# Optimization experiments

Measured on AMD Instinct MI355X. Metric: run time of the kernel, lower is better.

The kernel has to match this reference:

```python
import jax, jax.numpy as jnp
import numpy as np

N = 100000   # nodes
E = 1600000  # edges
F_IN = 256   # input features
H = 128      # hidden
C = 40       # classes


def setup_inputs() -> dict:
    key = jax.random.key(0)
    ks = jax.random.split(key, 6)
    x = jax.random.normal(ks[0], (N, F_IN), dtype=jnp.float32)
    edge_index = jax.random.randint(ks[1], (2, E), 0, N, dtype=jnp.int32)
    edge_attr = jax.random.uniform(ks[2], (E,), dtype=jnp.float32)
    # Glorot-style init like GCNConv
    W1 = jax.random.normal(ks[3], (F_IN, H), dtype=jnp.float32) * (1.0 / np.sqrt(F_IN))
    b1 = jnp.zeros((H,), dtype=jnp.float32)
    W2 = jax.random.normal(ks[4], (H, C), dtype=jnp.float32) * (1.0 / np.sqrt(H))
    b2 = jnp.zeros((C,), dtype=jnp.float32)
    return {"x": x, "edge_index": edge_index, "edge_attr": edge_attr,
            "W1": W1, "b1": b1, "W2": W2, "b2": b2}


def _gcn_norm(edge_index, edge_weight, num_nodes):
    # PyG gcn_norm: add self-loops (weight 1), symmetric D^{-1/2} A D^{-1/2}
    row, col = edge_index[0], edge_index[1]
    loop = jnp.arange(num_nodes, dtype=row.dtype)
    row = jnp.concatenate([row, loop])
    col = jnp.concatenate([col, loop])
    ew = jnp.concatenate([edge_weight, jnp.ones((num_nodes,), edge_weight.dtype)])
    deg = jax.ops.segment_sum(ew, col, num_segments=num_nodes)
    dinv = jnp.where(deg > 0, jax.lax.rsqrt(deg), 0.0)
    norm = dinv[row] * ew * dinv[col]
    return row, col, norm


def _gcn_conv(x, row, col, norm, W, b):
    h = x @ W                              # [N, out] dense transform first
    msg = h[row] * norm[:, None]           # gather source + edge scaling
    out = jax.ops.segment_sum(msg, col, num_segments=x.shape[0])  # scatter-add
    return out + b


def reference(x, edge_index, edge_attr, W1, b1, W2, b2):
    row, col, norm = _gcn_norm(edge_index, edge_attr, x.shape[0])
    h = _gcn_conv(x, row, col, norm, W1, b1)
    h = jax.nn.relu(h)
    # dropout is identity in eval mode
    h = _gcn_conv(h, row, col, norm, W2, b2)
    return jax.nn.log_softmax(h, axis=1)
```

## Files before the change

kernel.cpp:

```cpp
#include <hip/hip_runtime.h>

#define N_NODES 100000
#define N_EDGES 1600000
#define F_INPUT 256
#define H_DIM   128
#define C_DIM   40
#define NBKT    391
#define NCHK    1563
#define NMEGA   (2 * NCHK)

typedef short  bf8   __attribute__((ext_vector_type(8)));
typedef float  f32x4 __attribute__((ext_vector_type(4)));
typedef float  f32x2 __attribute__((ext_vector_type(2)));
typedef unsigned short u16x8 __attribute__((ext_vector_type(8)));

static __device__ __forceinline__ unsigned short f2bf(float f) {
    union { float f; unsigned u; } v; v.f = f;
    unsigned r = v.u + 0x7FFFu + ((v.u >> 16) & 1u);
    return (unsigned short)(r >> 16);
}
static __device__ __forceinline__ f32x2 bfpair(unsigned u) {
    union { unsigned u; float f; } lo, hi;
    lo.u = u << 16; hi.u = u & 0xFFFF0000u;
    return (f32x2){lo.f, hi.f};
}

__global__ void k_pre(const float* __restrict__ W1, const float* __restrict__ W2,
                      unsigned short* Wp1, unsigned short* Wp2) {
    int idx = blockIdx.x * 256 + threadIdx.x;
    if (idx < 32768) {
        int j = idx & 7, lane = (idx >> 3) & 63, ks = (idx >> 9) & 7, nt = idx >> 12;
        int m = lane & 15, q = lane >> 4;
        Wp1[idx] = f2bf(W1[(ks * 32 + q * 8 + j) * H_DIM + nt * 16 + m]);
    }
    int idx2 = idx - 32768;
    if (idx2 >= 0 && idx2 < 6144) {
        int j = idx2 & 7, lane = (idx2 >> 3) & 63, ks = (idx2 >> 9) & 3, nt = idx2 >> 11;
        int m = lane & 15, q = lane >> 4;
        int n = nt * 16 + m;
        Wp2[idx2] = (n < C_DIM) ? f2bf(W2[(ks * 32 + q * 8 + j) * C_DIM + n]) : (unsigned short)0;
    }
}

__global__ __launch_bounds__(256, 4) void k_mega2(
        const float* __restrict__ x, const unsigned short* __restrict__ Wp,
        unsigned short* __restrict__ h,
        const int* __restrict__ col, unsigned* __restrict__ histG) {
    __shared__ unsigned short lds_out[64 * H_DIM];
    int b = blockIdx.x;
    int tid = threadIdx.x;
    if (b & 1) {
        unsigned* histL = (unsigned*)lds_out;
        int chunk = b >> 1;
        for (int i = tid; i < NBKT; i += 256) histL[i] = 0;
        __syncthreads();
        int e0 = chunk * 1024 + tid;
#pragma unroll
        for (int k = 0; k < 4; k++) {
            int e = e0 + k * 256;
            if (e < N_EDGES) atomicAdd(&histL[col[e] >> 8], 1u);
        }
        __syncthreads();
        for (int i = tid; i < NBKT; i += 256) histG[(size_t)i * NCHK + chunk] = histL[i];
        return;
    }
    int tile = b >> 1;
    int wave = tid >> 6, lane = tid & 63;
    int m = lane & 15, q = lane >> 4;
    int row0 = tile * 64 + wave * 16;
    int rowA = row0 + m; if (rowA >= N_NODES) rowA = N_NODES - 1;

    f32x4 acc[8];
#pragma unroll
    for (int i = 0; i < 8; i++) acc[i] = (f32x4){0.f, 0.f, 0.f, 0.f};
    const float* xr = x + (long)rowA * F_INPUT + q * 8;
#pragma unroll
    for (int ks = 0; ks < 8; ks++) {
        float4 a0 = *(const float4*)(xr + ks * 32);
        float4 a1 = *(const float4*)(xr + ks * 32 + 4);
        bf8 a;
        a[0] = (short)f2bf(a0.x); a[1] = (short)f2bf(a0.y);
        a[2] = (short)f2bf(a0.z); a[3] = (short)f2bf(a0.w);
        a[4] = (short)f2bf(a1.x); a[5] = (short)f2bf(a1.y);
        a[6] = (short)f2bf(a1.z); a[7] = (short)f2bf(a1.w);
#pragma unroll
        for (int nt = 0; nt < 8; nt++) {
            bf8 bb = *(const bf8*)(Wp + (((nt * 8 + ks) * 64 + lane) << 3));
            acc[nt] = __builtin_amdgcn_mfma_f32_16x16x32_bf16(a, bb, acc[nt], 0, 0, 0);
        }
    }
    int lrow = wave * 16 + q * 4;
#pragma unroll
    for (int nt = 0; nt < 8; nt++)
#pragma unroll
        for (int r = 0; r < 4; r++)
            lds_out[(lrow + r) * H_DIM + nt * 16 + m] = f2bf(acc[nt][r]);
    __syncthreads();
    int valid = N_NODES - tile * 64; if (valid > 64) valid = 64;
    unsigned short* gbase = h + (size_t)tile * 64 * H_DIM;
#pragma unroll
    for (int i = 0; i < 4; i++) {
        int idx = (i * 256 + tid) * 8;
        if (idx < valid * H_DIM)
            *(u16x8*)(gbase + idx) = *(const u16x8*)(lds_out + idx);
    }
}

__global__ void k_scanB(unsigned* histG, unsigned* bktTotal) {
    __shared__ unsigned s[256];
    int B = blockIdx.x, t = threadIdx.x;
    unsigned carry = 0;
    for (int c0 = 0; c0 < NCHK; c0 += 256) {
        int idx = c0 + t;
        unsigned v = (idx < NCHK) ? histG[(size_t)B * NCHK + idx] : 0;
        s[t] = v; __syncthreads();
        for (int off = 1; off < 256; off <<= 1) {
            unsigned u = (t >= off) ? s[t - off] : 0;
            __syncthreads();
            s[t] += u;
            __syncthreads();
        }
        if (idx < NCHK) histG[(size_t)B * NCHK + idx] = s[t] - v + carry;
        unsigned tot = s[255];
        __syncthreads();
        carry += tot;
    }
    if (t == 0) bktTotal[B] = carry;
}

__global__ void k_scanC(const unsigned* __restrict__ bktTotal, unsigned* bucketBase) {
    __shared__ unsigned s[256];
    int t = threadIdx.x;
    unsigned carry = 0;
    for (int c0 = 0; c0 < NBKT; c0 += 256) {
        int idx = c0 + t;
        unsigned v = (idx < NBKT) ? bktTotal[idx] : 0;
        s[t] = v; __syncthreads();
        for (int off = 1; off < 256; off <<= 1) {
            unsigned u = (t >= off) ? s[t - off] : 0;
            __syncthreads();
            s[t] += u;
            __syncthreads();
        }
        if (idx < NBKT) bucketBase[idx] = s[t] - v + carry;
        unsigned tot = s[255];
        __syncthreads();
        carry += tot;
    }
    if (t == 0) bucketBase[NBKT] = carry;
}

__global__ void k_scat1(const int* __restrict__ row, const int* __restrict__ col,
                        const float* __restrict__ ea,
                        const unsigned* __restrict__ histG,
                        const unsigned* __restrict__ bucketBase,
                        int2* __restrict__ recs) {
    __shared__ unsigned base_l[NBKT];
    __shared__ unsigned cursor[NBKT];
    int blk = blockIdx.x, t = threadIdx.x;
    for (int i = t; i < NBKT; i += 256) {
        base_l[i] = bucketBase[i] + histG[(size_t)i * NCHK + blk];
        cursor[i] = 0;
    }
    __syncthreads();
    int e0 = blk * 1024 + t;
#pragma unroll
    for (int k = 0; k < 4; k++) {
        int e = e0 + k * 256;
        if (e < N_EDGES) {
            int c = col[e];
            int bkt = c >> 8;
            unsigned r = atomicAdd(&cursor[bkt], 1u);
            int pos = (int)(base_l[bkt] + r);
            recs[pos] = make_int2((row[e] << 8) | (c & 255), __float_as_int(ea[e]));
        }
    }
}

__global__ void k_pass2a(const int2* __restrict__ recs,
                         const unsigned* __restrict__ bucketBase,
                         int* __restrict__ start, int* __restrict__ cnt,
                         float* __restrict__ dinv) {
    __shared__ unsigned cntL[256];
    __shared__ unsigned wsL[256];
    __shared__ unsigned s[256];
    int B = blockIdx.x, t = threadIdx.x;
    cntL[t] = 0; wsL[t] = 0;
    __syncthreads();
    int lo = (int)bucketBase[B], hi = (int)bucketBase[B + 1];
    for (int i = lo + t; i < hi; i += 256) {
        int2 rc = recs[i];
        int cl = rc.x & 255;
        atomicAdd(&cntL[cl], 1u);
        unsigned q = __float2uint_rn(__int_as_float(rc.y) * 65536.0f);
        atomicAdd(&wsL[cl], q);
    }
    __syncthreads();
    unsigned v = cntL[t];
    s[t] = v; __syncthreads();
    for (int off = 1; off < 256; off <<= 1) {
        unsigned u = (t >= off) ? s[t - off] : 0;
        __syncthreads();
        s[t] += u;
        __syncthreads();
    }
    int node = B * 256 + t;
    if (node < N_NODES) {
        start[node] = (int)(bucketBase[B] + s[t] - v);
        cnt[node] = (int)v;
        dinv[node] = rsqrtf((float)(65536u + wsL[t]) * (1.0f / 65536.0f));
    }
}

__global__ void k_pass2b(const int2* __restrict__ recs,
                         const unsigned* __restrict__ bucketBase,
                         const int* __restrict__ start,
                         const float* __restrict__ dinv,
                         int2* __restrict__ csr) {
    __shared__ int startL[256];
    __shared__ unsigned cur[256];
    int B = blockIdx.x, t = threadIdx.x;
    int node = B * 256 + t;
    startL[t] = (node < N_NODES) ? start[node] : 0;
    cur[t] = 0;
    __syncthreads();
    int lo = (int)bucketBase[B], hi = (int)bucketBase[B + 1];
    for (int i = lo + t; i < hi; i += 256) {
        int2 rc = recs[i];
        int cl = rc.x & 255;
        int rw = rc.x >> 8;
        float w = __int_as_float(rc.y) * dinv[rw];
        unsigned r = atomicAdd(&cur[cl], 1u);
        csr[startL[cl] + (int)r] = make_int2(rw, __float_as_int(w));
    }
}

__global__ void k_agg1(const unsigned short* __restrict__ h, const int2* __restrict__ csr,
                       const int* __restrict__ start, const int* __restrict__ cnt,
                       const float* __restrict__ dinv, const float* __restrict__ b1,
                       unsigned short* __restrict__ h1) {
    int c = (blockIdx.x * blockDim.x + threadIdx.x) >> 6;
    int lane = threadIdx.x & 63;
    if (c >= N_NODES) return;
    int eg = lane >> 4, cl = lane & 15;
    float di = dinv[c];
    int s = start[c];
    int n = cnt[c];

    float w[5]; int r[5];
#pragma unroll
    for (int t = 0; t < 5; t++) {
        int i = eg + 4 * t;
        int2 p = csr[s + ((i < n) ? i : 0)];
        bool val = (i < n);
        r[t] = val ? p.x : c;
        w[t] = val ? __int_as_float(p.y) : 0.f;
    }
    uint4 gv[5];
#pragma unroll
    for (int t = 0; t < 5; t++)
        gv[t] = *(const uint4*)(h + (long)r[t] * H_DIM + cl * 8);
    uint4 selfv = (eg == 0) ? *(const uint4*)(h + (long)c * H_DIM + cl * 8)
                            : (uint4){0, 0, 0, 0};

    f32x2 acc[4];
#pragma unroll
    for (int k = 0; k < 4; k++) acc[k] = (f32x2){0.f, 0.f};
    {
        unsigned sv[4] = {selfv.x, selfv.y, selfv.z, selfv.w};
        f32x2 dd = (f32x2){di, di};
        if (eg == 0)
#pragma unroll
            for (int k = 0; k < 4; k++) acc[k] += dd * bfpair(sv[k]);
    }
#pragma unroll
    for (int t = 0; t < 5; t++) {
        unsigned vv[4] = {gv[t].x, gv[t].y, gv[t].z, gv[t].w};
        f32x2 ww = (f32x2){w[t], w[t]};
#pragma unroll
        for (int k = 0; k < 4; k++) acc[k] += ww * bfpair(vv[k]);
    }
    for (int i = 20 + eg; i < n; i += 4) {
        int2 p = csr[s + i];
        uint4 v4 = *(const uint4*)(h + (long)p.x * H_DIM + cl * 8);
        unsigned vv[4] = {v4.x, v4.y, v4.z, v4.w};
        float wt = __int_as_float(p.y);
        f32x2 ww = (f32x2){wt, wt};
#pragma unroll
        for (int k = 0; k < 4; k++) acc[k] += ww * bfpair(vv[k]);
    }
#pragma unroll
    for (int k = 0; k < 4; k++) {
        acc[k].x += __shfl_xor(acc[k].x, 16); acc[k].y += __shfl_xor(acc[k].y, 16);
        acc[k].x += __shfl_xor(acc[k].x, 32); acc[k].y += __shfl_xor(acc[k].y, 32);
    }
    if (eg == 0) {
        u16x8 o;
#pragma unroll
        for (int k = 0; k < 4; k++) {
            o[2 * k]     = f2bf(fmaxf(di * acc[k].x + b1[cl * 8 + 2 * k], 0.f));
            o[2 * k + 1] = f2bf(fmaxf(di * acc[k].y + b1[cl * 8 + 2 * k + 1], 0.f));
        }
        *(u16x8*)(h1 + (long)c * H_DIM + cl * 8) = o;
    }
}

__global__ __launch_bounds__(256, 4) void k_gemm2(const unsigned short* __restrict__ h1,
                        const unsigned short* __restrict__ Wp,
                        unsigned short* __restrict__ h2) {
    __shared__ unsigned short lds_out[64 * C_DIM];
    int tid = threadIdx.x;
    int wave = tid >> 6, lane = tid & 63;
    int m = lane & 15, q = lane >> 4;
    int row0 = blockIdx.x * 64 + wave * 16;
    int rowA = row0 + m; if (rowA >= N_NODES) rowA = N_NODES - 1;

    f32x4 acc[3];
#pragma unroll
    for (int i = 0; i < 3; i++) acc[i] = (f32x4){0.f, 0.f, 0.f, 0.f};
    const unsigned short* hr = h1 + (long)rowA * H_DIM + q * 8;
#pragma unroll
    for (int ks = 0; ks < 4; ks++) {
        bf8 a = *(const bf8*)(hr + ks * 32);
#pragma unroll
        for (int nt = 0; nt < 3; nt++) {
            bf8 b = *(const bf8*)(Wp + (((nt * 4 + ks) * 64 + lane) << 3));
            acc[nt] = __builtin_amdgcn_mfma_f32_16x16x32_bf16(a, b, acc[nt], 0, 0, 0);
        }
    }
    int lrow = wave * 16 + q * 4;
#pragma unroll
    for (int nt = 0; nt < 3; nt++)
#pragma unroll
        for (int r = 0; r < 4; r++) {
            int colo = nt * 16 + m;
            if (colo < C_DIM)
                lds_out[(lrow + r) * C_DIM + colo] = f2bf(acc[nt][r]);
        }
    __syncthreads();
    int valid = N_NODES - blockIdx.x * 64; if (valid > 64) valid = 64;
    unsigned short* gbase = h2 + (size_t)blockIdx.x * 64 * C_DIM;
    int total = valid * C_DIM;
#pragma unroll
    for (int i = 0; i < 3; i++) {
        int idx = (i * 256 + tid) * 4;
        if (idx < total)
            *(uint2*)(gbase + idx) = *(const uint2*)(lds_out + idx);
    }
}

__global__ void k_agg2(const unsigned short* __restrict__ h2, const int2* __restrict__ csr,
                       const int* __restrict__ start, const int* __restrict__ cnt,
                       const float* __restrict__ dinv, const float* __restrict__ b2,
                       float* __restrict__ out) {
    int c = (blockIdx.x * blockDim.x + threadIdx.x) >> 6;
    int lane = threadIdx.x & 63;
    if (c >= N_NODES) return;
    int eg = lane >> 3, cl = lane & 7;
    float di = dinv[c];
    int s = start[c];
    int n = cnt[c];

    float w[3]; int r[3];
#pragma unroll
    for (int t = 0; t < 3; t++) {
        int i = eg + 8 * t;
        int2 p = csr[s + ((i < n) ? i : 0)];
        bool val = (i < n);
        r[t] = val ? p.x : c;
        w[t] = val ? __int_as_float(p.y) : 0.f;
    }
    uint4 gv[3] = {{0,0,0,0},{0,0,0,0},{0,0,0,0}};
    uint4 selfv = {0, 0, 0, 0};
    if (cl < 5) {
#pragma unroll
        for (int t = 0; t < 3; t++)
            gv[t] = *(const uint4*)(h2 + (long)r[t] * C_DIM + cl * 8);
        if (eg == 0) selfv = *(const uint4*)(h2 + (long)c * C_DIM + cl * 8);
    }
    f32x2 acc[4];
#pragma unroll
    for (int k = 0; k < 4; k++) acc[k] = (f32x2){0.f, 0.f};
    {
        unsigned sv[4] = {selfv.x, selfv.y, selfv.z, selfv.w};
        f32x2 dd = (f32x2){di, di};
        if (eg == 0 && cl < 5)
#pragma unroll
            for (int k = 0; k < 4; k++) acc[k] += dd * bfpair(sv[k]);
    }
#pragma unroll
    for (int t = 0; t < 3; t++) {
        unsigned vv[4] = {gv[t].x, gv[t].y, gv[t].z, gv[t].w};
        f32x2 ww = (f32x2){w[t], w[t]};
#pragma unroll
        for (int k = 0; k < 4; k++) acc[k] += ww * bfpair(vv[k]);
    }
    for (int i = 24 + eg; i < n; i += 8) {
        int2 p = csr[s + i];
        if (cl < 5) {
            uint4 v4 = *(const uint4*)(h2 + (long)p.x * C_DIM + cl * 8);
            unsigned vv[4] = {v4.x, v4.y, v4.z, v4.w};
            float wt = __int_as_float(p.y);
            f32x2 ww = (f32x2){wt, wt};
#pragma unroll
            for (int k = 0; k < 4; k++) acc[k] += ww * bfpair(vv[k]);
        }
    }
#pragma unroll
    for (int k = 0; k < 4; k++) {
        acc[k].x += __shfl_xor(acc[k].x, 8);  acc[k].y += __shfl_xor(acc[k].y, 8);
        acc[k].x += __shfl_xor(acc[k].x, 16); acc[k].y += __shfl_xor(acc[k].y, 16);
        acc[k].x += __shfl_xor(acc[k].x, 32); acc[k].y += __shfl_xor(acc[k].y, 32);
    }
    float v[8];
    float lm = -INFINITY;
    if (cl < 5) {
#pragma unroll
        for (int k = 0; k < 4; k++) {
            v[2 * k]     = di * acc[k].x + b2[cl * 8 + 2 * k];
            v[2 * k + 1] = di * acc[k].y + b2[cl * 8 + 2 * k + 1];
            lm = fmaxf(lm, fmaxf(v[2 * k], v[2 * k + 1]));
        }
    }
    lm = fmaxf(lm, __shfl_xor(lm, 1));
    lm = fmaxf(lm, __shfl_xor(lm, 2));
    lm = fmaxf(lm, __shfl_xor(lm, 4));
    float ls = 0.f;
    if (cl < 5) {
#pragma unroll
        for (int j = 0; j < 8; j++) ls += __expf(v[j] - lm);
    }
    ls += __shfl_xor(ls, 1);
    ls += __shfl_xor(ls, 2);
    ls += __shfl_xor(ls, 4);
    if (eg == 0 && cl < 5) {
        float lsm = lm + logf(ls);
        f32x4 o0, o1;
#pragma unroll
        for (int j = 0; j < 4; j++) { o0[j] = v[j] - lsm; o1[j] = v[j + 4] - lsm; }
        *(f32x4*)(out + (long)c * C_DIM + cl * 8)     = o0;
        *(f32x4*)(out + (long)c * C_DIM + cl * 8 + 4) = o1;
    }
}

extern "C" void kernel_launch(void* const* d_in, const int* in_sizes, int n_in,
                              void* d_out, int out_size, void* d_ws, size_t ws_size,
                              hipStream_t stream) {
    const float* x  = (const float*)d_in[0];
    const int*   ei = (const int*)d_in[1];
    const float* ea = (const float*)d_in[2];
    const float* W1 = (const float*)d_in[3];
    const float* b1 = (const float*)d_in[4];
    const float* W2 = (const float*)d_in[5];
    const float* b2 = (const float*)d_in[6];
    const int* row = ei;
    const int* col = ei + N_EDGES;

    char* ws = (char*)d_ws;
    size_t off = 0;
    auto alloc = [&](size_t bytes) -> void* {
        void* p = ws + off;
        off = (off + bytes + 255) & ~(size_t)255;
        return p;
    };
    unsigned*       histG   = (unsigned*)alloc((size_t)NBKT * NCHK * 4);
    unsigned*       bktTot  = (unsigned*)alloc((size_t)NBKT * 4);
    unsigned*       bktBase = (unsigned*)alloc((size_t)(NBKT + 1) * 4);
    int*            start   = (int*)alloc((size_t)N_NODES * 4);
    int*            cnt     = (int*)alloc((size_t)N_NODES * 4);
    float*          dinv    = (float*)alloc((size_t)N_NODES * 4);
    int2*           recs    = (int2*)alloc((size_t)N_EDGES * 8);
    int2*           csr     = (int2*)alloc((size_t)N_EDGES * 8);
    unsigned short* Wp1     = (unsigned short*)alloc(32768 * 2);
    unsigned short* Wp2     = (unsigned short*)alloc(6144 * 2);
    unsigned short* h       = (unsigned short*)alloc((size_t)(N_NODES + 64) * H_DIM * 2);
    unsigned short* h1      = (unsigned short*)alloc((size_t)N_NODES * H_DIM * 2);
    unsigned short* h2      = (unsigned short*)alloc((size_t)(N_NODES + 64) * C_DIM * 2);

    k_pre<<<152, 256, 0, stream>>>(W1, W2, Wp1, Wp2);
    k_mega2<<<NMEGA, 256, 0, stream>>>(x, Wp1, h, col, histG);
    k_scanB<<<NBKT, 256, 0, stream>>>(histG, bktTot);
    k_scanC<<<1, 256, 0, stream>>>(bktTot, bktBase);
    k_scat1<<<NCHK, 256, 0, stream>>>(row, col, ea, histG, bktBase, recs);
    k_pass2a<<<NBKT, 256, 0, stream>>>(recs, bktBase, start, cnt, dinv);
    k_pass2b<<<NBKT, 256, 0, stream>>>(recs, bktBase, start, dinv, csr);
    k_agg1<<<N_NODES / 4, 256, 0, stream>>>(h, csr, start, cnt, dinv, b1, h1);
    k_gemm2<<<(N_NODES + 63) / 64, 256, 0, stream>>>(h1, Wp2, h2);
    k_agg2<<<N_NODES / 4, 256, 0, stream>>>(h2, csr, start, cnt, dinv, b2, (float*)d_out);
}
```

Before: 408.3 us.

## Split fused GEMM/histogram kernel and stage W1 in LDS with prefetched x

Splits the combined GEMM1+histogram kernel into separate histogram and GEMM launches. The GEMM kernel now copies the whole packed W1 (64 KB) into shared memory per block and issues all x loads for the tile up front before the MFMA loop. The aim is to cut repeated global/L2 reads of the weights and to expose more memory-level parallelism for x. In exchange it adds an extra launch, loses the overlap of histogram work with GEMM, and lowers occupancy because of the larger LDS footprint (launch bounds changed to 2).

```diff
diff --git a/kernel.cpp b/kernel.cpp
--- a/kernel.cpp
+++ b/kernel.cpp
@@ -7,7 +7,7 @@
 #define C_DIM   40
 #define NBKT    391
 #define NCHK    1563
-#define NMEGA   (2 * NCHK)
+#define NGEMM1  1563
 
 typedef short  bf8   __attribute__((ext_vector_type(8)));
 typedef float  f32x4 __attribute__((ext_vector_type(4)));
@@ -42,42 +42,53 @@
     }
 }
 
-__global__ __launch_bounds__(256, 4) void k_mega2(
+__global__ void k_hist(const int* __restrict__ col, unsigned* __restrict__ histG) {
+    __shared__ unsigned histL[NBKT];
+    int chunk = blockIdx.x, tid = threadIdx.x;
+    for (int i = tid; i < NBKT; i += 256) histL[i] = 0;
+    __syncthreads();
+    int e0 = chunk * 1024 + tid;
+#pragma unroll
+    for (int k = 0; k < 4; k++) {
+        int e = e0 + k * 256;
+        if (e < N_EDGES) atomicAdd(&histL[col[e] >> 8], 1u);
+    }
+    __syncthreads();
+    for (int i = tid; i < NBKT; i += 256) histG[(size_t)i * NCHK + chunk] = histL[i];
+}
+
+__global__ __launch_bounds__(256, 2) void k_gemm1(
         const float* __restrict__ x, const unsigned short* __restrict__ Wp,
-        unsigned short* __restrict__ h,
-        const int* __restrict__ col, unsigned* __restrict__ histG) {
+        unsigned short* __restrict__ h) {
+    __shared__ unsigned short sWp[32768];
     __shared__ unsigned short lds_out[64 * H_DIM];
-    int b = blockIdx.x;
     int tid = threadIdx.x;
-    if (b & 1) {
-        unsigned* histL = (unsigned*)lds_out;
-        int chunk = b >> 1;
-        for (int i = tid; i < NBKT; i += 256) histL[i] = 0;
-        __syncthreads();
-        int e0 = chunk * 1024 + tid;
-#pragma unroll
-        for (int k = 0; k < 4; k++) {
-            int e = e0 + k * 256;
-            if (e < N_EDGES) atomicAdd(&histL[col[e] >> 8], 1u);
-        }
-        __syncthreads();
-        for (int i = tid; i < NBKT; i += 256) histG[(size_t)i * NCHK + chunk] = histL[i];
-        return;
-    }
-    int tile = b >> 1;
     int wave = tid >> 6, lane = tid & 63;
     int m = lane & 15, q = lane >> 4;
+    int tile = blockIdx.x;
     int row0 = tile * 64 + wave * 16;
     int rowA = row0 + m; if (rowA >= N_NODES) rowA = N_NODES - 1;
+    const float* xr = x + (long)rowA * F_INPUT + q * 8;
+
+    float4 xv[16];
+#pragma unroll
+    for (int ks = 0; ks < 8; ks++) {
+        xv[2 * ks]     = *(const float4*)(xr + ks * 32);
+        xv[2 * ks + 1] = *(const float4*)(xr + ks * 32 + 4);
+    }
+#pragma unroll
+    for (int it = 0; it < 16; it++) {
+        int idx = (it * 256 + tid) * 8;
+        *(u16x8*)(sWp + idx) = *(const u16x8*)(Wp + idx);
+    }
+    __syncthreads();
 
     f32x4 acc[8];
 #pragma unroll
     for (int i = 0; i < 8; i++) acc[i] = (f32x4){0.f, 0.f, 0.f, 0.f};
-    const float* xr = x + (long)rowA * F_INPUT + q * 8;
 #pragma unroll
     for (int ks = 0; ks < 8; ks++) {
-        float4 a0 = *(const float4*)(xr + ks * 32);
-        float4 a1 = *(const float4*)(xr + ks * 32 + 4);
+        float4 a0 = xv[2 * ks], a1 = xv[2 * ks + 1];
         bf8 a;
         a[0] = (short)f2bf(a0.x); a[1] = (short)f2bf(a0.y);
         a[2] = (short)f2bf(a0.z); a[3] = (short)f2bf(a0.w);
@@ -85,7 +96,7 @@
         a[6] = (short)f2bf(a1.z); a[7] = (short)f2bf(a1.w);
 #pragma unroll
         for (int nt = 0; nt < 8; nt++) {
-            bf8 bb = *(const bf8*)(Wp + (((nt * 8 + ks) * 64 + lane) << 3));
+            bf8 bb = *(const bf8*)(sWp + (((nt * 8 + ks) * 64 + lane) << 3));
             acc[nt] = __builtin_amdgcn_mfma_f32_16x16x32_bf16(a, bb, acc[nt], 0, 0, 0);
         }
     }
@@ -478,7 +489,8 @@
     unsigned short* h2      = (unsigned short*)alloc((size_t)(N_NODES + 64) * C_DIM * 2);
 
     k_pre<<<152, 256, 0, stream>>>(W1, W2, Wp1, Wp2);
-    k_mega2<<<NMEGA, 256, 0, stream>>>(x, Wp1, h, col, histG);
+    k_hist<<<NCHK, 256, 0, stream>>>(col, histG);
+    k_gemm1<<<NGEMM1, 256, 0, stream>>>(x, Wp1, h);
     k_scanB<<<NBKT, 256, 0, stream>>>(histG, bktTot);
     k_scanC<<<1, 256, 0, stream>>>(bktTot, bktBase);
     k_scat1<<<NCHK, 256, 0, stream>>>(row, col, ea, histG, bktBase, recs);
```

Measured after the change: 372.1 us. 1.1x faster.
